# Performance work log

Measured on AMD Instinct MI355X. Metric: run time of the kernel, lower is better.

The kernel has to match this reference:

```python
import jax, jax.numpy as jnp
import numpy as np

B, M, E, D = 8, 8192, 2048, 64  # batch, nodes, hyperedges, feature dim (in_feats == out_feats required by the einsum)


def setup_inputs() -> dict:
    key = jax.random.key(0)
    k1, k2, k3, k4, k5 = jax.random.split(key, 5)
    inc_mat = (jax.random.uniform(k1, (B, M, E)) < 0.02).astype(jnp.float32)
    edge_features = jax.random.normal(k2, (B, E, D), dtype=jnp.float32)
    prev_node_features = jax.random.normal(k3, (B, M, D), dtype=jnp.float32)
    scale = 1.0 / np.sqrt(D)
    Wa = jax.random.normal(k4, (D, D), dtype=jnp.float32) * scale  # attention Linear weight (out, in)
    Wp = jax.random.normal(k5, (D, D), dtype=jnp.float32) * scale  # projection Linear weight (out, in)
    alpha = jnp.float32(0.5)
    return {"inc_mat": inc_mat, "edge_features": edge_features,
            "prev_node_features": prev_node_features, "Wa": Wa, "Wp": Wp, "alpha": alpha}


def reference(inc_mat, edge_features, prev_node_features, Wa, Wp, alpha):
    # edge_attention_scores = attention(edge_features): (b, e, d)
    edge_scores = jnp.einsum('bed,od->beo', edge_features, Wa)
    # node_attention_scores = bmm(inc_mat, edge_scores): (b, m, d)
    node_scores = jnp.einsum('bme,bed->bmd', inc_mat, edge_scores)
    # softmax over the node dim (dim=1 in torch)
    attn = jax.nn.softmax(node_scores, axis=1)
    # einsum('bed,bme->bmed') followed by einsum('bmed,bmd->bmd') reduces exactly to
    # (inc_mat @ edge_features) * attn — attention weights are independent of e.
    agg = jnp.einsum('bme,bed->bmd', inc_mat, edge_features)
    weighted = agg * attn
    node_features = jnp.einsum('bmd,od->bmo', weighted, Wp)
    return alpha * prev_node_features + (1.0 - alpha) * node_features
```

## Files before the change

kernel.cpp:

```cpp
#include <hip/hip_runtime.h>

#define NB 8
#define NM 8192
#define NE 2048
#define ND 64

typedef unsigned long long u64;
typedef unsigned short u16;
typedef float f32x4 __attribute__((ext_vector_type(4)));

constexpr int CAP     = 128;
constexpr int K1_ROWS = 32;
constexpr int K1_NBLK = NM / K1_ROWS;
constexpr int K4_ROWS = 64;
constexpr int K4_NBLK = NM / K4_ROWS;
constexpr int NROWS   = NB * NM;

__device__ __forceinline__ float bcast(float v, int d) {
    return __uint_as_float(__builtin_amdgcn_readlane(__float_as_uint(v), d));
}

__global__ __launch_bounds__(256) void k0_pack(const float* __restrict__ inc,
                                               u16* __restrict__ lists,
                                               int* __restrict__ counts) {
    const int lane = threadIdx.x & 63;
    const int gw   = (int)((blockIdx.x * 256u + threadIdx.x) >> 6);
    const int nw   = (int)((gridDim.x * 256u) >> 6);
    for (int row = gw; row < NROWS; row += nw) {
        const f32x4* rp = reinterpret_cast<const f32x4*>(inc + (size_t)row * NE);
        f32x4 v[8];
        #pragma unroll
        for (int c = 0; c < 8; ++c)
            v[c] = __builtin_nontemporal_load(rp + c * 64 + lane);

        u16* lst = lists + (size_t)row * CAP;
        int base = 0;
        #pragma unroll
        for (int c = 0; c < 8; ++c) {
            #pragma unroll
            for (int q = 0; q < 4; ++q) {
                const float x = v[c][q];
                u64 m = __ballot(x != 0.f);
                int below = __builtin_amdgcn_mbcnt_hi((unsigned)(m >> 32),
                            __builtin_amdgcn_mbcnt_lo((unsigned)m, 0));
                int pos = base + below;
                if (x != 0.f && pos < CAP)
                    lst[pos] = (u16)(c * 256 + lane * 4 + q);
                base += __popcll(m);
            }
        }
        if (lane == 0) counts[row] = base < CAP ? base : CAP;
    }
}

__global__ __launch_bounds__(256) void k1_gather(
    const u16* __restrict__ lists,
    const int* __restrict__ counts,
    const float* __restrict__ ef,
    const float* __restrict__ Wa,
    float* __restrict__ agg,
    float* __restrict__ score,
    float* __restrict__ pmax,
    float* __restrict__ psum)
{
    __shared__ float smax[4][ND];
    __shared__ float ssum[4][ND];

    const int tid  = threadIdx.x;
    const int lane = tid & 63;
    const int wave = tid >> 6;
    const int b    = blockIdx.x & 7;
    const int blk  = blockIdx.x >> 3;

    float wa[ND];
    #pragma unroll
    for (int k = 0; k < ND / 4; ++k) {
        f32x4 t = reinterpret_cast<const f32x4*>(Wa + (size_t)lane * ND)[k];
        wa[4 * k] = t.x; wa[4 * k + 1] = t.y; wa[4 * k + 2] = t.z; wa[4 * k + 3] = t.w;
    }

    const float* efb = ef + (size_t)b * (NE * ND);

    float runmax = -INFINITY, runsum = 0.f;

    for (int r = 0; r < K1_ROWS / 4; ++r) {
        const int m   = blk * K1_ROWS + r * 4 + wave;
        const int row = b * NM + m;
        const int cnt = counts[row];
        const unsigned pw = __builtin_nontemporal_load(
            reinterpret_cast<const unsigned*>(lists + (size_t)row * CAP) + lane);

        float a0 = 0.f, a1 = 0.f, a2 = 0.f, a3 = 0.f,
              a4 = 0.f, a5 = 0.f, a6 = 0.f, a7 = 0.f;
        int i = 0;
        for (; i + 8 <= cnt; i += 8) {
            const int h = i >> 1;
            unsigned w0 = __shfl(pw, h),     w1 = __shfl(pw, h + 1);
            unsigned w2 = __shfl(pw, h + 2), w3 = __shfl(pw, h + 3);
            a0 += efb[(size_t)(w0 & 0xffffu) * ND + lane];
            a1 += efb[(size_t)(w0 >> 16)     * ND + lane];
            a2 += efb[(size_t)(w1 & 0xffffu) * ND + lane];
            a3 += efb[(size_t)(w1 >> 16)     * ND + lane];
            a4 += efb[(size_t)(w2 & 0xffffu) * ND + lane];
            a5 += efb[(size_t)(w2 >> 16)     * ND + lane];
            a6 += efb[(size_t)(w3 & 0xffffu) * ND + lane];
            a7 += efb[(size_t)(w3 >> 16)     * ND + lane];
        }
        for (; i < cnt; ++i) {
            unsigned w = __shfl(pw, i >> 1);
            unsigned idx = (i & 1) ? (w >> 16) : (w & 0xffffu);
            a0 += efb[(size_t)idx * ND + lane];
        }
        const float acc = ((a0 + a1) + (a2 + a3)) + ((a4 + a5) + (a6 + a7));

        const size_t ro = ((size_t)b * NM + m) * ND;
        __builtin_nontemporal_store(acc, agg + ro + lane);

        float s = 0.f;
        #pragma unroll
        for (int d = 0; d < ND; ++d)
            s = fmaf(bcast(acc, d), wa[d], s);
        __builtin_nontemporal_store(s, score + ro + lane);

        float nm = fmaxf(runmax, s);
        runsum = runsum * __expf(runmax - nm) + __expf(s - nm);
        runmax = nm;
    }

    smax[wave][lane] = runmax;
    ssum[wave][lane] = runsum;
    __syncthreads();
    if (wave == 0) {
        float gm = smax[0][lane], gs = ssum[0][lane];
        for (int w = 1; w < 4; ++w) {
            float wm = smax[w][lane], ws = ssum[w][lane];
            float nm = fmaxf(gm, wm);
            gs = gs * __expf(gm - nm) + ws * __expf(wm - nm);
            gm = nm;
        }
        pmax[((size_t)b * K1_NBLK + blk) * ND + lane] = gm;
        psum[((size_t)b * K1_NBLK + blk) * ND + lane] = gs;
    }
}

__global__ __launch_bounds__(256) void k3_combine(
    const float* __restrict__ pmax, const float* __restrict__ psum,
    float* __restrict__ gmaxv, float* __restrict__ gsumv)
{
    __shared__ float smax[4][ND], ssum[4][ND];
    const int b = blockIdx.x, d = threadIdx.x & 63, c = threadIdx.x >> 6;
    float gm = -INFINITY, gs = 0.f;
    for (int i = c; i < K1_NBLK; i += 4) {
        float wm = pmax[((size_t)b * K1_NBLK + i) * ND + d];
        float ws = psum[((size_t)b * K1_NBLK + i) * ND + d];
        float nm = fmaxf(gm, wm);
        gs = gs * __expf(gm - nm) + ws * __expf(wm - nm);
        gm = nm;
    }
    smax[c][d] = gm; ssum[c][d] = gs;
    __syncthreads();
    if (c == 0) {
        for (int w = 1; w < 4; ++w) {
            float wm = smax[w][d], ws = ssum[w][d];
            float nm = fmaxf(gm, wm);
            gs = gs * __expf(gm - nm) + ws * __expf(wm - nm);
            gm = nm;
        }
        gmaxv[b * ND + d] = gm;
        gsumv[b * ND + d] = gs;
    }
}

__global__ __launch_bounds__(256) void k4_final(
    const float* __restrict__ agg, const float* __restrict__ score,
    const float* __restrict__ Wp, const float* __restrict__ prev,
    const float* __restrict__ gmaxv, const float* __restrict__ gsumv,
    const float* __restrict__ alpha_p, float* __restrict__ out)
{
    const int tid = threadIdx.x, lane = tid & 63, wave = tid >> 6;
    const int b = blockIdx.x / K4_NBLK, blk = blockIdx.x % K4_NBLK;

    float wp[ND];
    #pragma unroll
    for (int k = 0; k < ND / 4; ++k) {
        f32x4 t = reinterpret_cast<const f32x4*>(Wp + (size_t)lane * ND)[k];
        wp[4 * k] = t.x; wp[4 * k + 1] = t.y; wp[4 * k + 2] = t.z; wp[4 * k + 3] = t.w;
    }

    const float alpha = alpha_p[0];
    const float gmax = gmaxv[b * ND + lane];
    const float inv  = 1.0f / gsumv[b * ND + lane];

    for (int r = 0; r < K4_ROWS / 4; ++r) {
        const int m = blk * K4_ROWS + r * 4 + wave;
        const size_t ro = ((size_t)b * NM + m) * ND;
        const float a = __builtin_nontemporal_load(agg + ro + lane);
        const float s = __builtin_nontemporal_load(score + ro + lane);

        const float attn = __expf(s - gmax) * inv;
        const float w = a * attn;

        float nf = 0.f;
        #pragma unroll
        for (int d = 0; d < ND; ++d)
            nf = fmaf(bcast(w, d), wp[d], nf);

        const float pv = __builtin_nontemporal_load(prev + ro + lane);
        __builtin_nontemporal_store(alpha * pv + (1.f - alpha) * nf, out + ro + lane);
    }
}

extern "C" void kernel_launch(void* const* d_in, const int* in_sizes, int n_in,
                              void* d_out, int out_size, void* d_ws, size_t ws_size,
                              hipStream_t stream) {
    const float* inc     = (const float*)d_in[0];
    const float* ef      = (const float*)d_in[1];
    const float* prev    = (const float*)d_in[2];
    const float* Wa      = (const float*)d_in[3];
    const float* Wp      = (const float*)d_in[4];
    const float* alpha_p = (const float*)d_in[5];
    float* out = (float*)d_out;

    float* agg   = (float*)d_ws;
    float* scorev= agg   + (size_t)NB * NM * ND;
    float* pmax  = scorev+ (size_t)NB * NM * ND;
    float* psum  = pmax  + (size_t)NB * K1_NBLK * ND;
    float* gmaxv = psum  + (size_t)NB * K1_NBLK * ND;
    float* gsumv = gmaxv + NB * ND;
    int*   counts = (int*)(gsumv + NB * ND);
    u16*   lists  = (u16*)(counts + NROWS);

    k0_pack  <<<2048, 256, 0, stream>>>(inc, lists, counts);
    k1_gather<<<2048, 256, 0, stream>>>(lists, counts, ef, Wa, agg, scorev, pmax, psum);
    k3_combine<<<NB, 256, 0, stream>>>(pmax, psum, gmaxv, gsumv);
    k4_final <<<NB * K4_NBLK, 256, 0, stream>>>(agg, scorev, Wp, prev, gmaxv, gsumv, alpha_p, out);
}
```

Before: 232.6 us.

## Fuse incidence packing into gather kernel via per-wave LDS index lists

Merges the packing kernel, which compacts the nonzero column indices of each incidence row, into the gather kernel. Each wave now packs its own row into a shared-memory list and reads that list back right away, instead of writing index lists and counts to global memory and reading them in a second launch. This removes one kernel launch and the global round trip of the lists. In exchange, the dense incidence streaming and the dependent gather now run back to back inside the same wave, which may cut latency overlap.

```diff
diff --git a/kernel.cpp b/kernel.cpp
--- a/kernel.cpp
+++ b/kernel.cpp
@@ -10,52 +10,17 @@
 typedef float f32x4 __attribute__((ext_vector_type(4)));
 
 constexpr int CAP     = 128;
-constexpr int K1_ROWS = 32;
-constexpr int K1_NBLK = NM / K1_ROWS;
+constexpr int F0_ROWS = 32;
+constexpr int F0_NBLK = NM / F0_ROWS;
 constexpr int K4_ROWS = 64;
 constexpr int K4_NBLK = NM / K4_ROWS;
-constexpr int NROWS   = NB * NM;
 
 __device__ __forceinline__ float bcast(float v, int d) {
     return __uint_as_float(__builtin_amdgcn_readlane(__float_as_uint(v), d));
 }
 
-__global__ __launch_bounds__(256) void k0_pack(const float* __restrict__ inc,
-                                               u16* __restrict__ lists,
-                                               int* __restrict__ counts) {
-    const int lane = threadIdx.x & 63;
-    const int gw   = (int)((blockIdx.x * 256u + threadIdx.x) >> 6);
-    const int nw   = (int)((gridDim.x * 256u) >> 6);
-    for (int row = gw; row < NROWS; row += nw) {
-        const f32x4* rp = reinterpret_cast<const f32x4*>(inc + (size_t)row * NE);
-        f32x4 v[8];
-        #pragma unroll
-        for (int c = 0; c < 8; ++c)
-            v[c] = __builtin_nontemporal_load(rp + c * 64 + lane);
-
-        u16* lst = lists + (size_t)row * CAP;
-        int base = 0;
-        #pragma unroll
-        for (int c = 0; c < 8; ++c) {
-            #pragma unroll
-            for (int q = 0; q < 4; ++q) {
-                const float x = v[c][q];
-                u64 m = __ballot(x != 0.f);
-                int below = __builtin_amdgcn_mbcnt_hi((unsigned)(m >> 32),
-                            __builtin_amdgcn_mbcnt_lo((unsigned)m, 0));
-                int pos = base + below;
-                if (x != 0.f && pos < CAP)
-                    lst[pos] = (u16)(c * 256 + lane * 4 + q);
-                base += __popcll(m);
-            }
-        }
-        if (lane == 0) counts[row] = base < CAP ? base : CAP;
-    }
-}
-
-__global__ __launch_bounds__(256) void k1_gather(
-    const u16* __restrict__ lists,
-    const int* __restrict__ counts,
+__global__ __launch_bounds__(256) void f0_fused(
+    const float* __restrict__ inc,
     const float* __restrict__ ef,
     const float* __restrict__ Wa,
     float* __restrict__ agg,
@@ -63,6 +28,7 @@
     float* __restrict__ pmax,
     float* __restrict__ psum)
 {
+    __shared__ u16  packbuf[4][CAP];
     __shared__ float smax[4][ND];
     __shared__ float ssum[4][ND];
 
@@ -80,15 +46,39 @@
     }
 
     const float* efb = ef + (size_t)b * (NE * ND);
+    u16* const lst = packbuf[wave];
 
     float runmax = -INFINITY, runsum = 0.f;
 
-    for (int r = 0; r < K1_ROWS / 4; ++r) {
-        const int m   = blk * K1_ROWS + r * 4 + wave;
+    for (int r = 0; r < F0_ROWS / 4; ++r) {
+        const int m   = blk * F0_ROWS + r * 4 + wave;
         const int row = b * NM + m;
-        const int cnt = counts[row];
-        const unsigned pw = __builtin_nontemporal_load(
-            reinterpret_cast<const unsigned*>(lists + (size_t)row * CAP) + lane);
+
+        const f32x4* rp = reinterpret_cast<const f32x4*>(inc + (size_t)row * NE);
+        f32x4 v[8];
+        #pragma unroll
+        for (int c = 0; c < 8; ++c)
+            v[c] = __builtin_nontemporal_load(rp + c * 64 + lane);
+
+        int base = 0;
+        #pragma unroll
+        for (int c = 0; c < 8; ++c) {
+            #pragma unroll
+            for (int q = 0; q < 4; ++q) {
+                const float x = v[c][q];
+                u64 mb = __ballot(x != 0.f);
+                int below = __builtin_amdgcn_mbcnt_hi((unsigned)(mb >> 32),
+                            __builtin_amdgcn_mbcnt_lo((unsigned)mb, 0));
+                int pos = base + below;
+                if (x != 0.f && pos < CAP)
+                    lst[pos] = (u16)(c * 256 + lane * 4 + q);
+                base += __popcll(mb);
+            }
+        }
+        const int cnt = base < CAP ? base : CAP;
+
+        asm volatile("s_waitcnt lgkmcnt(0)" ::: "memory");
+        const unsigned pw = reinterpret_cast<const unsigned*>(lst)[lane];
 
         float a0 = 0.f, a1 = 0.f, a2 = 0.f, a3 = 0.f,
               a4 = 0.f, a5 = 0.f, a6 = 0.f, a7 = 0.f;
@@ -138,8 +128,8 @@
             gs = gs * __expf(gm - nm) + ws * __expf(wm - nm);
             gm = nm;
         }
-        pmax[((size_t)b * K1_NBLK + blk) * ND + lane] = gm;
-        psum[((size_t)b * K1_NBLK + blk) * ND + lane] = gs;
+        pmax[((size_t)b * F0_NBLK + blk) * ND + lane] = gm;
+        psum[((size_t)b * F0_NBLK + blk) * ND + lane] = gs;
     }
 }
 
@@ -150,9 +140,9 @@
     __shared__ float smax[4][ND], ssum[4][ND];
     const int b = blockIdx.x, d = threadIdx.x & 63, c = threadIdx.x >> 6;
     float gm = -INFINITY, gs = 0.f;
-    for (int i = c; i < K1_NBLK; i += 4) {
-        float wm = pmax[((size_t)b * K1_NBLK + i) * ND + d];
-        float ws = psum[((size_t)b * K1_NBLK + i) * ND + d];
+    for (int i = c; i < F0_NBLK; i += 4) {
+        float wm = pmax[((size_t)b * F0_NBLK + i) * ND + d];
+        float ws = psum[((size_t)b * F0_NBLK + i) * ND + d];
         float nm = fmaxf(gm, wm);
         gs = gs * __expf(gm - nm) + ws * __expf(wm - nm);
         gm = nm;
@@ -224,14 +214,11 @@
     float* agg   = (float*)d_ws;
     float* scorev= agg   + (size_t)NB * NM * ND;
     float* pmax  = scorev+ (size_t)NB * NM * ND;
-    float* psum  = pmax  + (size_t)NB * K1_NBLK * ND;
-    float* gmaxv = psum  + (size_t)NB * K1_NBLK * ND;
+    float* psum  = pmax  + (size_t)NB * F0_NBLK * ND;
+    float* gmaxv = psum  + (size_t)NB * F0_NBLK * ND;
     float* gsumv = gmaxv + NB * ND;
-    int*   counts = (int*)(gsumv + NB * ND);
-    u16*   lists  = (u16*)(counts + NROWS);
-
-    k0_pack  <<<2048, 256, 0, stream>>>(inc, lists, counts);
-    k1_gather<<<2048, 256, 0, stream>>>(lists, counts, ef, Wa, agg, scorev, pmax, psum);
+
+    f0_fused <<<NB * F0_NBLK, 256, 0, stream>>>(inc, ef, Wa, agg, scorev, pmax, psum);
     k3_combine<<<NB, 256, 0, stream>>>(pmax, psum, gmaxv, gsumv);
     k4_final <<<NB * K4_NBLK, 256, 0, stream>>>(agg, scorev, Wp, prev, gmaxv, gsumv, alpha_p, out);
 }
```

Measured after the change: 210.6 us. 9.4% less time.
